# Kernel tuning notes

Measured on AMD Instinct MI355X. Metric: run time of the kernel, lower is better.

## Reference

```python
import jax, jax.numpy as jnp
import numpy as np

SCALE = 20.0
THRESHOLD = 0.9995


def setup_inputs() -> dict:
    key = jax.random.key(0)
    k1, k2, k3 = jax.random.split(key, 3)
    B, C, H, W, S = 4, 128, 96, 128, 1024
    # L2-normalize along channel so the dot product is a true cosine in [-1, 1]
    # (keeps exp(scale * (x - threshold)) numerically sane, as intended by the module).
    def unit(x):
        return x / (jnp.linalg.norm(x, axis=1, keepdims=True) + 1e-8)
    source_feature_map = unit(jax.random.normal(k1, (B, C, H, W), dtype=jnp.float32))
    target_feature_map = unit(jax.random.normal(k2, (B, C, H, W), dtype=jnp.float32))
    source_feature_1D_locations = jax.random.randint(k3, (B, S, 1), 0, H * W, dtype=jnp.int64)
    mask = jnp.ones((B, 1, H, W), dtype=jnp.float32)
    return {
        "source_feature_map": source_feature_map,
        "target_feature_map": target_feature_map,
        "source_feature_1D_locations": source_feature_1D_locations,
        "mask": mask,
    }


def reference(source_feature_map, target_feature_map, source_feature_1D_locations, mask):
    B, C, H, W = source_feature_map.shape
    loc = source_feature_1D_locations[..., 0]  # [B, S]
    src_flat = source_feature_map.reshape(B, C, H * W)  # [B, C, HW]
    # gather sampled query vectors: [B, C, S]
    sampled = jnp.take_along_axis(src_flat, loc[:, None, :], axis=2)
    # per-batch 1x1 conv == batched matmul: [B, S, H, W]
    corr = jnp.einsum('bchw,bcs->bshw', target_feature_map, sampled)
    resp = jnp.exp(SCALE * (0.5 * corr + 0.5 - THRESHOLD)) * mask  # mask broadcasts [B,1,H,W]
    resp = resp / jnp.sum(resp, axis=(2, 3), keepdims=True)
    return resp
```

## Files before the change

### kernel.cpp

```cpp
#include <hip/hip_runtime.h>

typedef unsigned int u32;
typedef unsigned short u16;
typedef short s8v __attribute__((ext_vector_type(8)));
typedef float f16v __attribute__((ext_vector_type(16)));

#define NB 4
#define NC 128
#define HW 12288
#define NS 1024

#define EXP_A 10.0f
#define EXP_B (-9.99f)

#define TS 256
#define TP 256
#define NPT (HW/TP)
#define NST (NS/TS)

__device__ inline u16 f2bf(float f) {
    u32 u = __float_as_uint(f);
    return (u16)((u + 0x7fffu + ((u >> 16) & 1u)) >> 16);
}
__device__ inline float bf2f(u16 h) { return __uint_as_float(((u32)h) << 16); }

__device__ inline void gload_lds16(const void* g, void* l) {
    __builtin_amdgcn_global_load_lds(
        (const __attribute__((address_space(1))) void*)g,
        (__attribute__((address_space(3))) void*)l, 16, 0, 0);
}

__global__ __launch_bounds__(256) void prep_samp(
    const float* __restrict__ src, const int* __restrict__ loc,
    u16* __restrict__ ahi, u16* __restrict__ alo, float* __restrict__ sums)
{
    int t = threadIdx.x;
    int gid = blockIdx.x * 256 + t;
    if (gid < NB * NS) sums[gid] = 0.0f;
    int bs = blockIdx.x * 2 + (t >> 7);
    int c  = t & 127;
    int b  = bs >> 10, s = bs & 1023;
    int l  = loc[bs];
    float v = src[((size_t)(b * NC + c)) * HW + l];
    u16 h  = f2bf(v);
    u16 lo = f2bf(v - bf2f(h));
    int kc = c >> 5, u = (c >> 3) & 3, e = c & 7;
    int slot = u ^ ((s >> 1) & 3);
    size_t off = ((size_t)((b * 4 + kc) * NS + s)) * 32 + slot * 8 + e;
    ahi[off] = h;
    alo[off] = lo;
}

__global__ __launch_bounds__(256) void prep_tgt(
    const float* __restrict__ tgt, u16* __restrict__ bhi, u16* __restrict__ blo)
{
    int b = blockIdx.y, pt = blockIdx.x, t = threadIdx.x;
    int pxl = t & 63, u = t >> 6;
    int px = pt * 64 + pxl;
    int slot = u ^ ((px >> 1) & 3);
#pragma unroll
    for (int kc = 0; kc < 4; ++kc) {
        int c0 = kc * 32 + u * 8;
        u32 hq[4], lq[4];
#pragma unroll
        for (int k = 0; k < 4; ++k) {
            float v0 = tgt[((size_t)(b * NC + c0 + 2 * k)) * HW + px];
            float v1 = tgt[((size_t)(b * NC + c0 + 2 * k + 1)) * HW + px];
            u16 h0 = f2bf(v0), h1 = f2bf(v1);
            u16 l0 = f2bf(v0 - bf2f(h0)), l1 = f2bf(v1 - bf2f(h1));
            hq[k] = (u32)h0 | ((u32)h1 << 16);
            lq[k] = (u32)l0 | ((u32)l1 << 16);
        }
        size_t off = (((size_t)((b * 4 + kc) * HW + px)) * 4 + slot) * 8;
        *(uint4*)(bhi + off) = make_uint4(hq[0], hq[1], hq[2], hq[3]);
        *(uint4*)(blo + off) = make_uint4(lq[0], lq[1], lq[2], lq[3]);
    }
}

template <int DO_STORE>
__global__ __launch_bounds__(512) void corr2(
    const u16* __restrict__ bhi, const u16* __restrict__ blo,
    const u16* __restrict__ ahi, const u16* __restrict__ alo,
    const float* __restrict__ mask, float* __restrict__ sums,
    float* __restrict__ out)
{
    __shared__ __align__(1024) char sm[65536];
    __shared__ float inv[TS];

    int f = blockIdx.x;
    int xcd = f & 7, r0 = f >> 3;
    int st = r0 & 3;
    int p  = (r0 >> 2) * 8 + xcd;
    int b  = p / 48, pt = p - b * 48;

    int t = threadIdx.x, w = t >> 6, l = t & 63, ln = l & 31, h = l >> 5;
    int ws = w >> 1, wp = w & 1;

    if (DO_STORE) {
        if (t < TS) inv[t] = 1.0f / sums[b * NS + st * TS + t];
    }

    f16v acc[2][4];
#pragma unroll
    for (int i = 0; i < 2; ++i)
#pragma unroll
        for (int j = 0; j < 4; ++j)
#pragma unroll
            for (int r = 0; r < 16; ++r) acc[i][j][r] = 0.0f;

    for (int kc = 0; kc < 4; ++kc) {
        const char* ga_h = (const char*)ahi + ((size_t)((b * 4 + kc) * NS + st * TS)) * 64;
        const char* ga_l = (const char*)alo + ((size_t)((b * 4 + kc) * NS + st * TS)) * 64;
        const char* gb_h = (const char*)bhi + ((size_t)((b * 4 + kc) * HW + pt * TP)) * 64;
        const char* gb_l = (const char*)blo + ((size_t)((b * 4 + kc) * HW + pt * TP)) * 64;
#pragma unroll
        for (int it = 0; it < 8; ++it) {
            int q = w * 8 + it;
            int rg = q >> 4, inner = q & 15;
            const char* gb = rg == 0 ? ga_h : rg == 1 ? ga_l : rg == 2 ? gb_h : gb_l;
            gload_lds16(gb + inner * 1024 + l * 16, sm + q * 1024);
        }
        __syncthreads();

#pragma unroll
        for (int kk2 = 0; kk2 < 2; ++kk2) {
            int u = kk2 * 2 + h;
            s8v a_h[2], a_l[2], b_h[4], b_l[4];
#pragma unroll
            for (int i = 0; i < 2; ++i) {
                int row = ws * 64 + i * 32 + ln;
                int sl = u ^ ((row >> 1) & 3);
                a_h[i] = *(const s8v*)(sm + 0 * 16384 + row * 64 + sl * 16);
                a_l[i] = *(const s8v*)(sm + 1 * 16384 + row * 64 + sl * 16);
            }
#pragma unroll
            for (int j = 0; j < 4; ++j) {
                int px = wp * 128 + j * 32 + ln;
                int sl = u ^ ((px >> 1) & 3);
                b_h[j] = *(const s8v*)(sm + 2 * 16384 + px * 64 + sl * 16);
                b_l[j] = *(const s8v*)(sm + 3 * 16384 + px * 64 + sl * 16);
            }
#pragma unroll
            for (int i = 0; i < 2; ++i)
#pragma unroll
                for (int j = 0; j < 4; ++j) {
                    acc[i][j] = __builtin_amdgcn_mfma_f32_32x32x16_bf16(a_h[i], b_h[j], acc[i][j], 0, 0, 0);
                    acc[i][j] = __builtin_amdgcn_mfma_f32_32x32x16_bf16(a_l[i], b_h[j], acc[i][j], 0, 0, 0);
                    acc[i][j] = __builtin_amdgcn_mfma_f32_32x32x16_bf16(a_h[i], b_l[j], acc[i][j], 0, 0, 0);
                }
        }
        __syncthreads();
    }

    float mv[4];
#pragma unroll
    for (int j = 0; j < 4; ++j)
        mv[j] = mask[(size_t)b * HW + pt * TP + wp * 128 + j * 32 + ln];

    if (DO_STORE) {
        float* ob0 = out + ((size_t)(b * NS + st * TS)) * HW + pt * TP + wp * 128 + ln;
#pragma unroll
        for (int i = 0; i < 2; ++i) {
            int rb = ws * 64 + i * 32 + 4 * h;
#pragma unroll
            for (int j = 0; j < 4; ++j) {
#pragma unroll
                for (int r = 0; r < 16; ++r) {
                    int row = rb + (r & 3) + 8 * (r >> 2);
                    float e = __expf(fmaf(acc[i][j][r], EXP_A, EXP_B)) * mv[j];
                    ob0[(size_t)row * HW + j * 32] = e * inv[row];
                }
            }
        }
    } else {
        float* rs = (float*)sm;
#pragma unroll
        for (int i = 0; i < 2; ++i) {
            int rb = ws * 64 + i * 32 + 4 * h;
#pragma unroll
            for (int r = 0; r < 16; ++r) {
                int row = rb + (r & 3) + 8 * (r >> 2);
                float e = 0.0f;
#pragma unroll
                for (int j = 0; j < 4; ++j)
                    e += __expf(fmaf(acc[i][j][r], EXP_A, EXP_B)) * mv[j];
                rs[(wp * TS + row) * 32 + ln] = e;
            }
        }
        __syncthreads();
        int row = t & 255, half = t >> 8;
        float tot = 0.0f;
#pragma unroll
        for (int c = 0; c < 32; ++c)
            tot += rs[(half * TS + row) * 32 + ((c + t) & 31)];
        atomicAdd(&sums[b * NS + st * TS + row], tot);
    }
}

extern "C" void kernel_launch(void* const* d_in, const int* in_sizes, int n_in,
                              void* d_out, int out_size, void* d_ws, size_t ws_size,
                              hipStream_t stream) {
    const float* src  = (const float*)d_in[0];
    const float* tgt  = (const float*)d_in[1];
    const int*   loc  = (const int*)d_in[2];
    const float* mask = (const float*)d_in[3];
    float* out = (float*)d_out;

    char* ws = (char*)d_ws;
    const size_t BPLANE = (size_t)NB * 4 * HW * 32 * sizeof(u16);
    const size_t APLANE = (size_t)NB * 4 * NS * 32 * sizeof(u16);
    u16* bhi = (u16*)ws;
    u16* blo = (u16*)(ws + BPLANE);
    u16* ahi = (u16*)(ws + 2 * BPLANE);
    u16* alo = (u16*)(ws + 2 * BPLANE + APLANE);
    float* sums = (float*)(ws + 2 * BPLANE + 2 * APLANE);

    prep_samp<<<dim3(NB * NS / 2), 256, 0, stream>>>(src, loc, ahi, alo, sums);
    prep_tgt<<<dim3(HW / 64, NB), 256, 0, stream>>>(tgt, bhi, blo);

    dim3 g(NPT * NST * NB);
    corr2<0><<<g, 512, 0, stream>>>(bhi, blo, ahi, alo, mask, sums, out);
    corr2<1><<<g, 512, 0, stream>>>(bhi, blo, ahi, alo, mask, sums, out);
}
```

Measured before the change: 324.8 us.

## Fuse sum and store passes into one GEMM pass plus rescale kernel

```diff
diff --git a/kernel.cpp b/kernel.cpp
--- a/kernel.cpp
+++ b/kernel.cpp
@@ -30,62 +30,62 @@
         (__attribute__((address_space(3))) void*)l, 16, 0, 0);
 }
 
-__global__ __launch_bounds__(256) void prep_samp(
-    const float* __restrict__ src, const int* __restrict__ loc,
-    u16* __restrict__ ahi, u16* __restrict__ alo, float* __restrict__ sums)
+__global__ __launch_bounds__(256) void prep(
+    const float* __restrict__ src, const float* __restrict__ tgt,
+    const int* __restrict__ loc,
+    u16* __restrict__ ahi, u16* __restrict__ alo,
+    u16* __restrict__ bhi, u16* __restrict__ blo,
+    float* __restrict__ sums)
 {
-    int t = threadIdx.x;
-    int gid = blockIdx.x * 256 + t;
-    if (gid < NB * NS) sums[gid] = 0.0f;
-    int bs = blockIdx.x * 2 + (t >> 7);
-    int c  = t & 127;
-    int b  = bs >> 10, s = bs & 1023;
-    int l  = loc[bs];
-    float v = src[((size_t)(b * NC + c)) * HW + l];
-    u16 h  = f2bf(v);
-    u16 lo = f2bf(v - bf2f(h));
-    int kc = c >> 5, u = (c >> 3) & 3, e = c & 7;
-    int slot = u ^ ((s >> 1) & 3);
-    size_t off = ((size_t)((b * 4 + kc) * NS + s)) * 32 + slot * 8 + e;
-    ahi[off] = h;
-    alo[off] = lo;
-}
-
-__global__ __launch_bounds__(256) void prep_tgt(
-    const float* __restrict__ tgt, u16* __restrict__ bhi, u16* __restrict__ blo)
-{
-    int b = blockIdx.y, pt = blockIdx.x, t = threadIdx.x;
-    int pxl = t & 63, u = t >> 6;
-    int px = pt * 64 + pxl;
-    int slot = u ^ ((px >> 1) & 3);
-#pragma unroll
-    for (int kc = 0; kc < 4; ++kc) {
-        int c0 = kc * 32 + u * 8;
-        u32 hq[4], lq[4];
-#pragma unroll
-        for (int k = 0; k < 4; ++k) {
-            float v0 = tgt[((size_t)(b * NC + c0 + 2 * k)) * HW + px];
-            float v1 = tgt[((size_t)(b * NC + c0 + 2 * k + 1)) * HW + px];
-            u16 h0 = f2bf(v0), h1 = f2bf(v1);
-            u16 l0 = f2bf(v0 - bf2f(h0)), l1 = f2bf(v1 - bf2f(h1));
-            hq[k] = (u32)h0 | ((u32)h1 << 16);
-            lq[k] = (u32)l0 | ((u32)l1 << 16);
-        }
-        size_t off = (((size_t)((b * 4 + kc) * HW + px)) * 4 + slot) * 8;
-        *(uint4*)(bhi + off) = make_uint4(hq[0], hq[1], hq[2], hq[3]);
-        *(uint4*)(blo + off) = make_uint4(lq[0], lq[1], lq[2], lq[3]);
-    }
-}
-
-template <int DO_STORE>
-__global__ __launch_bounds__(512) void corr2(
+    int blk = blockIdx.x, t = threadIdx.x;
+    if (blk < (HW / 64) * NB) {
+        int b = blk / (HW / 64), pt = blk - b * (HW / 64);
+        int pxl = t & 63, u = t >> 6;
+        int px = pt * 64 + pxl;
+        int slot = u ^ ((px >> 1) & 3);
+#pragma unroll
+        for (int kc = 0; kc < 4; ++kc) {
+            int c0 = kc * 32 + u * 8;
+            u32 hq[4], lq[4];
+#pragma unroll
+            for (int k = 0; k < 4; ++k) {
+                float v0 = tgt[((size_t)(b * NC + c0 + 2 * k)) * HW + px];
+                float v1 = tgt[((size_t)(b * NC + c0 + 2 * k + 1)) * HW + px];
+                u16 h0 = f2bf(v0), h1 = f2bf(v1);
+                u16 l0 = f2bf(v0 - bf2f(h0)), l1 = f2bf(v1 - bf2f(h1));
+                hq[k] = (u32)h0 | ((u32)h1 << 16);
+                lq[k] = (u32)l0 | ((u32)l1 << 16);
+            }
+            size_t off = (((size_t)((b * 4 + kc) * HW + px)) * 4 + slot) * 8;
+            *(uint4*)(bhi + off) = make_uint4(hq[0], hq[1], hq[2], hq[3]);
+            *(uint4*)(blo + off) = make_uint4(lq[0], lq[1], lq[2], lq[3]);
+        }
+    } else {
+        int sb = blk - (HW / 64) * NB;
+        int gid = sb * 256 + t;
+        if (gid < NB * NS) sums[gid] = 0.0f;
+        int bs = sb * 2 + (t >> 7);
+        int c  = t & 127;
+        int b  = bs >> 10, s = bs & 1023;
+        int l  = loc[bs];
+        float v = src[((size_t)(b * NC + c)) * HW + l];
+        u16 h  = f2bf(v);
+        u16 lo = f2bf(v - bf2f(h));
+        int kc = c >> 5, u = (c >> 3) & 3, e = c & 7;
+        int slot = u ^ ((s >> 1) & 3);
+        size_t off = ((size_t)((b * 4 + kc) * NS + s)) * 32 + slot * 8 + e;
+        ahi[off] = h;
+        alo[off] = lo;
+    }
+}
+
+__global__ __launch_bounds__(512) void corr_fused(
     const u16* __restrict__ bhi, const u16* __restrict__ blo,
     const u16* __restrict__ ahi, const u16* __restrict__ alo,
     const float* __restrict__ mask, float* __restrict__ sums,
     float* __restrict__ out)
 {
     __shared__ __align__(1024) char sm[65536];
-    __shared__ float inv[TS];
 
     int f = blockIdx.x;
     int xcd = f & 7, r0 = f >> 3;
@@ -96,10 +96,6 @@
     int t = threadIdx.x, w = t >> 6, l = t & 63, ln = l & 31, h = l >> 5;
     int ws = w >> 1, wp = w & 1;
 
-    if (DO_STORE) {
-        if (t < TS) inv[t] = 1.0f / sums[b * NS + st * TS + t];
-    }
-
     f16v acc[2][4];
 #pragma unroll
     for (int i = 0; i < 2; ++i)
@@ -140,6 +136,7 @@
                 b_h[j] = *(const s8v*)(sm + 2 * 16384 + px * 64 + sl * 16);
                 b_l[j] = *(const s8v*)(sm + 3 * 16384 + px * 64 + sl * 16);
             }
+            __builtin_amdgcn_s_setprio(1);
 #pragma unroll
             for (int i = 0; i < 2; ++i)
 #pragma unroll
@@ -148,6 +145,7 @@
                     acc[i][j] = __builtin_amdgcn_mfma_f32_32x32x16_bf16(a_l[i], b_h[j], acc[i][j], 0, 0, 0);
                     acc[i][j] = __builtin_amdgcn_mfma_f32_32x32x16_bf16(a_h[i], b_l[j], acc[i][j], 0, 0, 0);
                 }
+            __builtin_amdgcn_s_setprio(0);
         }
         __syncthreads();
     }
@@ -157,43 +155,45 @@
     for (int j = 0; j < 4; ++j)
         mv[j] = mask[(size_t)b * HW + pt * TP + wp * 128 + j * 32 + ln];
 
-    if (DO_STORE) {
-        float* ob0 = out + ((size_t)(b * NS + st * TS)) * HW + pt * TP + wp * 128 + ln;
-#pragma unroll
-        for (int i = 0; i < 2; ++i) {
-            int rb = ws * 64 + i * 32 + 4 * h;
+    float* rs = (float*)sm;
+    float* ob0 = out + ((size_t)(b * NS + st * TS)) * HW + pt * TP + wp * 128 + ln;
+#pragma unroll
+    for (int i = 0; i < 2; ++i) {
+        int rb = ws * 64 + i * 32 + 4 * h;
+#pragma unroll
+        for (int r = 0; r < 16; ++r) {
+            int row = rb + (r & 3) + 8 * (r >> 2);
+            float tot = 0.0f;
 #pragma unroll
             for (int j = 0; j < 4; ++j) {
-#pragma unroll
-                for (int r = 0; r < 16; ++r) {
-                    int row = rb + (r & 3) + 8 * (r >> 2);
-                    float e = __expf(fmaf(acc[i][j][r], EXP_A, EXP_B)) * mv[j];
-                    ob0[(size_t)row * HW + j * 32] = e * inv[row];
-                }
-            }
-        }
-    } else {
-        float* rs = (float*)sm;
-#pragma unroll
-        for (int i = 0; i < 2; ++i) {
-            int rb = ws * 64 + i * 32 + 4 * h;
-#pragma unroll
-            for (int r = 0; r < 16; ++r) {
-                int row = rb + (r & 3) + 8 * (r >> 2);
-                float e = 0.0f;
-#pragma unroll
-                for (int j = 0; j < 4; ++j)
-                    e += __expf(fmaf(acc[i][j][r], EXP_A, EXP_B)) * mv[j];
-                rs[(wp * TS + row) * 32 + ln] = e;
-            }
-        }
-        __syncthreads();
-        int row = t & 255, half = t >> 8;
-        float tot = 0.0f;
-#pragma unroll
-        for (int c = 0; c < 32; ++c)
-            tot += rs[(half * TS + row) * 32 + ((c + t) & 31)];
-        atomicAdd(&sums[b * NS + st * TS + row], tot);
+                float e = __expf(fmaf(acc[i][j][r], EXP_A, EXP_B)) * mv[j];
+                ob0[(size_t)row * HW + j * 32] = e;
+                tot += e;
+            }
+            rs[(wp * TS + row) * 32 + ln] = tot;
+        }
+    }
+    __syncthreads();
+    int row2 = t & 255, half = t >> 8;
+    float tot = 0.0f;
+#pragma unroll
+    for (int c = 0; c < 32; ++c)
+        tot += rs[(half * TS + row2) * 32 + ((c + t) & 31)];
+    atomicAdd(&sums[b * NS + st * TS + row2], tot);
+}
+
+__global__ __launch_bounds__(256) void rescale(
+    const float* __restrict__ sums, float* __restrict__ out)
+{
+    int bs = blockIdx.x;
+    float inv = 1.0f / sums[bs];
+    float4* p = (float4*)(out + (size_t)bs * HW);
+    int t = threadIdx.x;
+#pragma unroll
+    for (int i = 0; i < 12; ++i) {
+        float4 v = p[t + i * 256];
+        v.x *= inv; v.y *= inv; v.z *= inv; v.w *= inv;
+        p[t + i * 256] = v;
     }
 }
 
@@ -215,10 +215,11 @@
     u16* alo = (u16*)(ws + 2 * BPLANE + APLANE);
     float* sums = (float*)(ws + 2 * BPLANE + 2 * APLANE);
 
-    prep_samp<<<dim3(NB * NS / 2), 256, 0, stream>>>(src, loc, ahi, alo, sums);
-    prep_tgt<<<dim3(HW / 64, NB), 256, 0, stream>>>(tgt, bhi, blo);
+    prep<<<dim3((HW / 64) * NB + NB * NS / 2), 256, 0, stream>>>(
+        src, tgt, loc, ahi, alo, bhi, blo, sums);
 
     dim3 g(NPT * NST * NB);
-    corr2<0><<<g, 512, 0, stream>>>(bhi, blo, ahi, alo, mask, sums, out);
-    corr2<1><<<g, 512, 0, stream>>>(bhi, blo, ahi, alo, mask, sums, out);
-}
+    corr_fused<<<g, 512, 0, stream>>>(bhi, blo, ahi, alo, mask, sums, out);
+
+    rescale<<<dim3(NB * NS), 256, 0, stream>>>(sums, out);
+}
```

Result: no change. 329.7 us (+1.5%).
